# Optimization experiments

Hardware: AMD Instinct MI355X
Metric: run time of the kernel (lower is better)

The kernel has to match this reference:

```python
import jax, jax.numpy as jnp
import numpy as np

# 7 axial hex directions (dy, dx) including center, matching HexConv2d.DIRS
DIRS = [(0, 0), (1, 0), (0, 1), (-1, 1), (-1, 0), (0, -1), (1, -1)]


def _shift(x, dy, dx):
    """torch.roll-style shift with zero fill at wrapped edges. x: [B,C,H,W]."""
    sx, sy = -dx, -dy
    y = jnp.roll(x, shift=(sy, sx), axis=(2, 3))
    if sy > 0:
        y = y.at[:, :, :sy, :].set(0)
    elif sy < 0:
        y = y.at[:, :, sy:, :].set(0)
    if sx > 0:
        y = y.at[:, :, :, :sx].set(0)
    elif sx < 0:
        y = y.at[:, :, :, sx:].set(0)
    return y


def _hex_mask(H, dtype):
    size = H // 2
    q = jnp.arange(-size, size + 1)
    Q, R = jnp.meshgrid(q, q, indexing='ij')
    S = -Q - R
    # |Q|<=size and |R|<=size hold by construction; only |S|<=size cuts corners
    mask = ((jnp.abs(Q) <= size) & (jnp.abs(R) <= size) & (jnp.abs(S) <= size))
    return mask.astype(dtype)[None, None]  # [1,1,H,W]


def setup_inputs() -> dict:
    key = jax.random.key(0)
    k1, k2, k3 = jax.random.split(key, 3)
    B, Cin, Cout, H = 32, 256, 256, 49
    x = jax.random.normal(k1, (B, Cin, H, H), dtype=jnp.float32)
    weight = jax.random.normal(k2, (Cout, Cin, 7), dtype=jnp.float32) * 0.02
    bias = jax.random.normal(k3, (Cout,), dtype=jnp.float32) * 0.02
    return {"x": x, "weight": weight, "bias": bias}


def reference(x, weight, bias):
    mask = _hex_mask(x.shape[2], x.dtype)          # [1,1,H,W]
    x = x * mask
    # [7,B,C,H,W]: shifted+masked neighbor maps
    nbr = jnp.stack([_shift(x, dy, dx) for (dy, dx) in DIRS], axis=0) * mask
    # fused 1x1 conv over (channel, direction): weight [O,C,7]
    y = jnp.einsum('nbchw,ocn->bohw', nbr, weight) + bias[None, :, None, None]
    return y * mask
```

## Files before the change

### kernel.cpp

```cpp
#include <hip/hip_runtime.h>


typedef __attribute__((ext_vector_type(8))) short short8;
typedef __attribute__((ext_vector_type(4))) short short4v;
typedef __attribute__((ext_vector_type(4))) float floatx4;

#define NPIX   2401
#define W50    50
#define PREAL  2450
#define XBLEAD 56
#define XBROWS 2672
#define PT3    128
#define NT3    20
#define NSEG3  15
#define BUFB   (NSEG3*1024)
#define XB3_BYTES ((size_t)32*XBROWS*256*2)
#define WP_BYTES  917504ULL
#define WS_NEED3  (XB3_BYTES + WP_BYTES)

__device__ __forceinline__ unsigned short f2bf(float f) {
  unsigned u = __builtin_bit_cast(unsigned, f);
  u += 0x7fffu + ((u >> 16) & 1u);
  return (unsigned short)(u >> 16);
}

__global__ void prep_w_kernel(const float* __restrict__ w, unsigned short* __restrict__ wp) {
  int t = blockIdx.x * 256 + threadIdx.x;
  int l  = t & 63;
  int ot = (t >> 6) & 15;
  int kc = (t >> 10) & 7;
  int n  = t >> 13;
  int o  = ot * 16 + (l & 15);
  int cb = kc * 32 + ((l >> 4) * 8);
  const float* src = w + (size_t)(o * 256 + cb) * 7 + n;
  short8 pk;
#pragma unroll
  for (int j = 0; j < 8; ++j) pk[j] = (short)f2bf(src[j * 7]);
  ((short8*)wp)[t] = pk;
}

__global__ void zero_pads(unsigned short* __restrict__ xb) {
  int idx = blockIdx.x * 256 + threadIdx.x;
  int c16 = idx & 31;
  int rb  = idx >> 5;
  int row = rb % XBROWS;
  int b   = rb / XBROWS;
  int p   = row - XBLEAD;
  bool pad = (p < 0) || (p >= PREAL) || (p % W50 == 49);
  if (pad) {
    short8 z = {0,0,0,0,0,0,0,0};
    *(short8*)(xb + ((size_t)b * XBROWS + row) * 256 + c16 * 8) = z;
  }
}

__global__ __launch_bounds__(256)
void prep_x3(const float* __restrict__ x, unsigned short* __restrict__ xb) {
  __shared__ unsigned short t[64][68];
  const int tid = threadIdx.x;
  const int span = blockIdx.x, cg = blockIdx.y, b = blockIdx.z;
  const int s0 = span * 64;
  {
    const int chl = tid >> 2, i4 = tid & 3;
    const float* src = x + ((size_t)(b * 256 + cg * 64 + chl)) * NPIX;
#pragma unroll
    for (int it = 0; it < 4; ++it) {
      int pxl = it * 16 + i4 * 4;
      int r = s0 + pxl;
      float vv[4] = {0.f, 0.f, 0.f, 0.f};
      if (r + 3 < NPIX) {
        float4 v = *(const float4*)(src + r);
        vv[0] = v.x; vv[1] = v.y; vv[2] = v.z; vv[3] = v.w;
      } else {
#pragma unroll
        for (int e = 0; e < 4; ++e) if (r + e < NPIX) vv[e] = src[r + e];
      }
      short4v u = {0, 0, 0, 0};
#pragma unroll
      for (int e = 0; e < 4; ++e) {
        int re = r + e;
        unsigned short uu = 0;
        if (re < NPIX) {
          int h = re / 49, w = re - h * 49, s = h + w;
          if (s >= 24 && s <= 72) uu = f2bf(vv[e]);
        }
        u[e] = (short)uu;
      }
      *(short4v*)&t[chl][pxl] = u;
    }
  }
  __syncthreads();
  const int rl = tid >> 2, cpart = tid & 3;
  const int r = s0 + rl;
  if (r < NPIX) {
    int p = r + r / 49;
    unsigned short* dst = xb + ((size_t)b * XBROWS + (p + XBLEAD)) * 256 + cg * 64 + cpart * 16;
    short8 o0, o1;
#pragma unroll
    for (int k = 0; k < 8; ++k) o0[k] = (short)t[cpart * 16 + k][rl];
#pragma unroll
    for (int k = 0; k < 8; ++k) o1[k] = (short)t[cpart * 16 + 8 + k][rl];
    *(short8*)dst = o0;
    *(short8*)(dst + 8) = o1;
  }
}

__global__ __launch_bounds__(256, 2)
void hexconv_v3(const unsigned short* __restrict__ xb,
                const unsigned short* __restrict__ wp,
                const float* __restrict__ bias,
                float* __restrict__ out) {
  __shared__ __attribute__((aligned(16))) unsigned char smem[2 * BUFB];

  const int tid  = threadIdx.x;
  const int lane = tid & 63;
  const int wv   = tid >> 6;
  const int col  = lane & 15;
  const int quad = lane >> 4;

  const int pt = blockIdx.x;
  const int b  = blockIdx.y;
  const int P0 = pt * PT3;
  const int phase = (pt + b * 3) & 7;

  const int OFF[7] = {0, 50, 1, -49, -50, -1, 49};

  int ba[7];
#pragma unroll
  for (int n = 0; n < 7; ++n) {
    int r0 = col + 56 + OFF[n];
    int r64 = r0 << 6;
    ba[n] = (r64 + quad * 16) ^ ((r64 >> 3) & 0x30);
  }

  const int gpart = (lane & 3) ^ ((lane >> 3) & 3);
  const char* gsrc0 = (const char*)(xb + ((size_t)b * XBROWS + (size_t)P0) * 256)
                      + (lane >> 2) * 512 + gpart * 16;

  auto stage = [&](int buf, int kc) {
    char* ldsb = (char*)smem + buf * BUFB;
    for (int s = wv; s < NSEG3; s += 4)
      __builtin_amdgcn_global_load_lds(
          (const __attribute__((address_space(1))) unsigned int*)(gsrc0 + (size_t)s * 8192 + kc * 64),
          (__attribute__((address_space(3))) unsigned int*)(ldsb + s * 1024), 16, 0, 0);
  };

  const char* wbase = (const char*)wp + (size_t)(wv * 4) * 1024 + lane * 16;
  auto loadA = [&](int kc, int n, short8* dst) {
#pragma unroll
    for (int ii = 0; ii < 4; ++ii)
      dst[ii] = *(const short8*)(wbase + ((size_t)((n * 8 + kc) * 16 + ii)) * 1024);
  };

  floatx4 acc[4][8];
#pragma unroll
  for (int ii = 0; ii < 4; ++ii)
#pragma unroll
    for (int j = 0; j < 8; ++j) acc[ii][j] = (floatx4){0.f, 0.f, 0.f, 0.f};

  stage(0, phase);
  short8 afc[4];
  loadA(phase, 0, afc);
  __syncthreads();

  for (int i = 0; i < 8; ++i) {
    const int kc  = (i + phase) & 7;
    const int kcn = (i + 1 + phase) & 7;
    if (i < 7) stage((i + 1) & 1, kcn);
    const char* bufp = (const char*)smem + (i & 1) * BUFB;
#pragma unroll
    for (int n = 0; n < 7; ++n) {
      short8 afn[4];
      loadA((n < 6) ? kc : kcn, (n < 6) ? n + 1 : 0, afn);
      short8 bf[8];
#pragma unroll
      for (int j = 0; j < 8; ++j)
        bf[j] = *(const short8*)(bufp + ba[n] + j * 1024);
#pragma unroll
      for (int ii = 0; ii < 4; ++ii)
#pragma unroll
        for (int j = 0; j < 8; ++j)
          acc[ii][j] = __builtin_amdgcn_mfma_f32_16x16x32_bf16(afc[ii], bf[j], acc[ii][j], 0, 0, 0);
#pragma unroll
      for (int ii = 0; ii < 4; ++ii) afc[ii] = afn[ii];
    }
    __syncthreads();
  }

  const int ob = wv * 64;
  floatx4 bv[4];
#pragma unroll
  for (int ii = 0; ii < 4; ++ii)
    bv[ii] = *(const floatx4*)(bias + ob + ii * 16 + quad * 4);

#pragma unroll
  for (int j = 0; j < 8; ++j) {
    int p = P0 + j * 16 + col;
    int h = p / W50;
    int w = p - h * W50;
    if (w >= 49 || p >= PREAL) continue;
    bool m = (h + w >= 24) && (h + w <= 72);
    size_t ridx = (size_t)h * 49 + w;
#pragma unroll
    for (int ii = 0; ii < 4; ++ii) {
      float* dst = out + ((size_t)(b * 256 + ob + ii * 16 + quad * 4)) * NPIX + ridx;
#pragma unroll
      for (int rr = 0; rr < 4; ++rr) {
        float v = m ? (acc[ii][j][rr] + bv[ii][rr]) : 0.f;
        dst[(size_t)rr * NPIX] = v;
      }
    }
  }
}

#define PITCH  40
#define V1WIN  168
#define V1ZROW 168
__global__ __launch_bounds__(256)
void hexconv_v1(const float* __restrict__ x,
                const unsigned short* __restrict__ wp,
                const float* __restrict__ bias,
                float* __restrict__ out) {
  __shared__ unsigned short sm[(V1ZROW + 2) * PITCH];
  const int tid = threadIdx.x, lane = tid & 63, wv = tid >> 6;
  const int col = lane & 15, quad = lane >> 4;
  const int pt = blockIdx.x, b = blockIdx.y;
  const int P0 = pt * 64, win_start = P0 - 52;
  if (tid < PITCH * 2) sm[V1ZROW * PITCH + tid] = 0;
  const int OFF[7] = {0, 49, 1, -48, -49, -1, 48};
  const int DXP = (1 << 2) | (1 << 3), DXN = (1 << 5) | (1 << 6);
  int baddr[4][7];
#pragma unroll
  for (int j = 0; j < 4; ++j) {
    int pix = P0 + j * 16 + col;
    int wj = pix % 49;
    int rowbase = pix - win_start;
#pragma unroll
    for (int n = 0; n < 7; ++n) {
      bool bad = (((DXP >> n) & 1) && wj == 48) || (((DXN >> n) & 1) && wj == 0);
      int row = bad ? V1ZROW : (rowbase + OFF[n]);
      baddr[j][n] = row * (PITCH * 2) + quad * 16;
    }
  }
  int sp[3], sgp[3]; bool sok[3];
#pragma unroll
  for (int pi = 0; pi < 3; ++pi) {
    int p = lane + pi * 64, gp = win_start + p;
    sp[pi] = p; sgp[pi] = gp;
    bool hm = false;
    if (gp >= 0 && gp < NPIX) { int h = gp / 49, w = gp - h * 49, s = h + w; hm = (s >= 24 && s <= 72); }
    sok[pi] = (p < V1WIN) && hm;
  }
  floatx4 acc[4][4];
#pragma unroll
  for (int i = 0; i < 4; ++i)
#pragma unroll
    for (int j = 0; j < 4; ++j) acc[i][j] = (floatx4){0.f, 0.f, 0.f, 0.f};
  const short8* wpv = (const short8*)wp;
  const int wslot = wv * 4;
  for (int kc = 0; kc < 8; ++kc) {
    __syncthreads();
#pragma unroll
    for (int ci = 0; ci < 8; ++ci) {
      int c = ci * 4 + wv;
      const float* src = x + ((size_t)(b * 256 + kc * 32 + c)) * NPIX;
#pragma unroll
      for (int pi = 0; pi < 3; ++pi) {
        if (sp[pi] < V1WIN) {
          float v = sok[pi] ? src[sgp[pi]] : 0.f;
          sm[sp[pi] * PITCH + c] = f2bf(v);
        }
      }
    }
    __syncthreads();
#pragma unroll
    for (int n = 0; n < 7; ++n) {
      short8 af[4];
#pragma unroll
      for (int i = 0; i < 4; ++i)
        af[i] = wpv[((size_t)((n * 8 + kc) * 16 + wslot + i)) * 64 + lane];
      short8 bf[4];
#pragma unroll
      for (int j = 0; j < 4; ++j)
        bf[j] = *(const short8*)((const char*)sm + baddr[j][n]);
#pragma unroll
      for (int i = 0; i < 4; ++i)
#pragma unroll
        for (int j = 0; j < 4; ++j)
          acc[i][j] = __builtin_amdgcn_mfma_f32_16x16x32_bf16(af[i], bf[j], acc[i][j], 0, 0, 0);
    }
  }
  const int ob = wv * 64;
  floatx4 bv[4];
#pragma unroll
  for (int i = 0; i < 4; ++i)
    bv[i] = *(const floatx4*)(bias + ob + i * 16 + quad * 4);
#pragma unroll
  for (int j = 0; j < 4; ++j) {
    int pix = P0 + j * 16 + col;
    if (pix >= NPIX) continue;
    int h = pix / 49, w = pix - h * 49;
    bool m = (h + w >= 24 && h + w <= 72);
#pragma unroll
    for (int i = 0; i < 4; ++i) {
      int o = ob + i * 16 + quad * 4;
      float* dst = out + ((size_t)(b * 256 + o)) * NPIX + pix;
#pragma unroll
      for (int r = 0; r < 4; ++r) {
        float v = m ? (acc[i][j][r] + bv[i][r]) : 0.f;
        dst[(size_t)r * NPIX] = v;
      }
    }
  }
}

extern "C" void kernel_launch(void* const* d_in, const int* in_sizes, int n_in,
                              void* d_out, int out_size, void* d_ws, size_t ws_size,
                              hipStream_t stream) {
  const float* x    = (const float*)d_in[0];
  const float* w    = (const float*)d_in[1];
  const float* bias = (const float*)d_in[2];
  float* out = (float*)d_out;

  if (ws_size >= WS_NEED3) {
    unsigned short* xb = (unsigned short*)d_ws;
    unsigned short* wp = (unsigned short*)((char*)d_ws + XB3_BYTES);
    zero_pads<<<(32 * XBROWS * 32) / 256, 256, 0, stream>>>(xb);
    prep_w_kernel<<<224, 256, 0, stream>>>(w, wp);
    prep_x3<<<dim3(38, 4, 32), 256, 0, stream>>>(x, xb);
    hexconv_v3<<<dim3(NT3, 32), 256, 0, stream>>>(xb, wp, bias, out);
  } else {
    unsigned short* wp = (unsigned short*)d_ws;
    prep_w_kernel<<<224, 256, 0, stream>>>(w, wp);
    hexconv_v1<<<dim3(38, 32), 256, 0, stream>>>(x, wp, bias, out);
  }
}
```

Baseline: 239.0 us.

## Halve pixel tile to 64, raise occupancy, and rework prep_x transpose stores

The main conv kernel now covers 64 pixels per block instead of 128, giving 39x32 blocks. It keeps a 4x4 accumulator set, uses a smaller LDS double buffer and sets launch bounds to 3 blocks per CU. The aim is better occupancy and load balance across CUs. The cost is more redundant loading of weight and halo data per output, and the removal of the weight register prefetch. The prep_x transpose also changes so each thread packs two pixels' 8-channel vectors from 32-bit LDS reads, which targets LDS bank conflicts and wider stores.

```diff
diff --git a/kernel.cpp b/kernel.cpp
--- a/kernel.cpp
+++ b/kernel.cpp
@@ -10,10 +10,9 @@
 #define PREAL  2450
 #define XBLEAD 56
 #define XBROWS 2672
-#define PT3    128
-#define NT3    20
-#define NSEG3  15
-#define BUFB   (NSEG3*1024)
+#define NT4    39
+#define NSEG4  11
+#define BUFB4  (NSEG4*1024)
 #define XB3_BYTES ((size_t)32*XBROWS*256*2)
 #define WP_BYTES  917504ULL
 #define WS_NEED3  (XB3_BYTES + WP_BYTES)
@@ -54,7 +53,7 @@
 }
 
 __global__ __launch_bounds__(256)
-void prep_x3(const float* __restrict__ x, unsigned short* __restrict__ xb) {
+void prep_x4(const float* __restrict__ x, unsigned short* __restrict__ xb) {
   __shared__ unsigned short t[64][68];
   const int tid = threadIdx.x;
   const int span = blockIdx.x, cg = blockIdx.y, b = blockIdx.z;
@@ -62,10 +61,10 @@
   {
     const int chl = tid >> 2, i4 = tid & 3;
     const float* src = x + ((size_t)(b * 256 + cg * 64 + chl)) * NPIX;
+    const int rbase = s0 + i4 * 16;
 #pragma unroll
     for (int it = 0; it < 4; ++it) {
-      int pxl = it * 16 + i4 * 4;
-      int r = s0 + pxl;
+      int r = rbase + it * 4;
       float vv[4] = {0.f, 0.f, 0.f, 0.f};
       if (r + 3 < NPIX) {
         float4 v = *(const float4*)(src + r);
@@ -85,31 +84,44 @@
         }
         u[e] = (short)uu;
       }
-      *(short4v*)&t[chl][pxl] = u;
+      *(short4v*)&t[chl][i4 * 16 + it * 4] = u;
     }
   }
   __syncthreads();
-  const int rl = tid >> 2, cpart = tid & 3;
-  const int r = s0 + rl;
-  if (r < NPIX) {
-    int p = r + r / 49;
-    unsigned short* dst = xb + ((size_t)b * XBROWS + (p + XBLEAD)) * 256 + cg * 64 + cpart * 16;
-    short8 o0, o1;
-#pragma unroll
-    for (int k = 0; k < 8; ++k) o0[k] = (short)t[cpart * 16 + k][rl];
-#pragma unroll
-    for (int k = 0; k < 8; ++k) o1[k] = (short)t[cpart * 16 + 8 + k][rl];
-    *(short8*)dst = o0;
-    *(short8*)(dst + 8) = o1;
-  }
-}
-
-__global__ __launch_bounds__(256, 2)
-void hexconv_v3(const unsigned short* __restrict__ xb,
+  const int pp = tid >> 3;
+  const int co = tid & 7;
+  unsigned d[8];
+#pragma unroll
+  for (int k = 0; k < 8; ++k) d[k] = *(const unsigned*)&t[co * 8 + k][pp * 2];
+  uint4 lo, hi;
+  {
+    unsigned l0[4], h0[4];
+#pragma unroll
+    for (int m = 0; m < 4; ++m) {
+      unsigned a = d[2 * m], bq = d[2 * m + 1];
+      l0[m] = (a & 0xffffu) | (bq << 16);
+      h0[m] = (a >> 16) | (bq & 0xffff0000u);
+    }
+    lo = make_uint4(l0[0], l0[1], l0[2], l0[3]);
+    hi = make_uint4(h0[0], h0[1], h0[2], h0[3]);
+  }
+  const int r_lo = s0 + pp * 2, r_hi = r_lo + 1;
+  if (r_lo < NPIX) {
+    int prow = r_lo + r_lo / 49 + XBLEAD;
+    *(uint4*)(xb + ((size_t)b * XBROWS + prow) * 256 + cg * 64 + co * 8) = lo;
+  }
+  if (r_hi < NPIX) {
+    int prow = r_hi + r_hi / 49 + XBLEAD;
+    *(uint4*)(xb + ((size_t)b * XBROWS + prow) * 256 + cg * 64 + co * 8) = hi;
+  }
+}
+
+__global__ __launch_bounds__(256, 3)
+void hexconv_v4(const unsigned short* __restrict__ xb,
                 const unsigned short* __restrict__ wp,
                 const float* __restrict__ bias,
                 float* __restrict__ out) {
-  __shared__ __attribute__((aligned(16))) unsigned char smem[2 * BUFB];
+  __shared__ __attribute__((aligned(16))) unsigned char smem[2 * BUFB4];
 
   const int tid  = threadIdx.x;
   const int lane = tid & 63;
@@ -119,7 +131,7 @@
 
   const int pt = blockIdx.x;
   const int b  = blockIdx.y;
-  const int P0 = pt * PT3;
+  const int P0 = pt * 64;
   const int phase = (pt + b * 3) & 7;
 
   const int OFF[7] = {0, 50, 1, -49, -50, -1, 49};
@@ -137,51 +149,44 @@
                       + (lane >> 2) * 512 + gpart * 16;
 
   auto stage = [&](int buf, int kc) {
-    char* ldsb = (char*)smem + buf * BUFB;
-    for (int s = wv; s < NSEG3; s += 4)
+    char* ldsb = (char*)smem + buf * BUFB4;
+    for (int s = wv; s < NSEG4; s += 4)
       __builtin_amdgcn_global_load_lds(
           (const __attribute__((address_space(1))) unsigned int*)(gsrc0 + (size_t)s * 8192 + kc * 64),
           (__attribute__((address_space(3))) unsigned int*)(ldsb + s * 1024), 16, 0, 0);
   };
 
   const char* wbase = (const char*)wp + (size_t)(wv * 4) * 1024 + lane * 16;
-  auto loadA = [&](int kc, int n, short8* dst) {
-#pragma unroll
-    for (int ii = 0; ii < 4; ++ii)
-      dst[ii] = *(const short8*)(wbase + ((size_t)((n * 8 + kc) * 16 + ii)) * 1024);
-  };
-
-  floatx4 acc[4][8];
+
+  floatx4 acc[4][4];
 #pragma unroll
   for (int ii = 0; ii < 4; ++ii)
 #pragma unroll
-    for (int j = 0; j < 8; ++j) acc[ii][j] = (floatx4){0.f, 0.f, 0.f, 0.f};
+    for (int j = 0; j < 4; ++j) acc[ii][j] = (floatx4){0.f, 0.f, 0.f, 0.f};
 
   stage(0, phase);
-  short8 afc[4];
-  loadA(phase, 0, afc);
   __syncthreads();
 
   for (int i = 0; i < 8; ++i) {
     const int kc  = (i + phase) & 7;
     const int kcn = (i + 1 + phase) & 7;
     if (i < 7) stage((i + 1) & 1, kcn);
-    const char* bufp = (const char*)smem + (i & 1) * BUFB;
+    const char* bufp = (const char*)smem + (i & 1) * BUFB4;
 #pragma unroll
     for (int n = 0; n < 7; ++n) {
-      short8 afn[4];
-      loadA((n < 6) ? kc : kcn, (n < 6) ? n + 1 : 0, afn);
-      short8 bf[8];
-#pragma unroll
-      for (int j = 0; j < 8; ++j)
+      short8 af[4];
+#pragma unroll
+      for (int ii = 0; ii < 4; ++ii)
+        af[ii] = *(const short8*)(wbase + ((size_t)((n * 8 + kc) * 16 + ii)) * 1024);
+      short8 bf[4];
+#pragma unroll
+      for (int j = 0; j < 4; ++j)
         bf[j] = *(const short8*)(bufp + ba[n] + j * 1024);
 #pragma unroll
       for (int ii = 0; ii < 4; ++ii)
 #pragma unroll
-        for (int j = 0; j < 8; ++j)
-          acc[ii][j] = __builtin_amdgcn_mfma_f32_16x16x32_bf16(afc[ii], bf[j], acc[ii][j], 0, 0, 0);
-#pragma unroll
-      for (int ii = 0; ii < 4; ++ii) afc[ii] = afn[ii];
+        for (int j = 0; j < 4; ++j)
+          acc[ii][j] = __builtin_amdgcn_mfma_f32_16x16x32_bf16(af[ii], bf[j], acc[ii][j], 0, 0, 0);
     }
     __syncthreads();
   }
@@ -193,7 +198,7 @@
     bv[ii] = *(const floatx4*)(bias + ob + ii * 16 + quad * 4);
 
 #pragma unroll
-  for (int j = 0; j < 8; ++j) {
+  for (int j = 0; j < 4; ++j) {
     int p = P0 + j * 16 + col;
     int h = p / W50;
     int w = p - h * W50;
@@ -326,8 +331,8 @@
     unsigned short* wp = (unsigned short*)((char*)d_ws + XB3_BYTES);
     zero_pads<<<(32 * XBROWS * 32) / 256, 256, 0, stream>>>(xb);
     prep_w_kernel<<<224, 256, 0, stream>>>(w, wp);
-    prep_x3<<<dim3(38, 4, 32), 256, 0, stream>>>(x, xb);
-    hexconv_v3<<<dim3(NT3, 32), 256, 0, stream>>>(xb, wp, bias, out);
+    prep_x4<<<dim3(38, 4, 32), 256, 0, stream>>>(x, xb);
+    hexconv_v4<<<dim3(NT4, 32), 256, 0, stream>>>(xb, wp, bias, out);
   } else {
     unsigned short* wp = (unsigned short*)d_ws;
     prep_w_kernel<<<224, 256, 0, stream>>>(w, wp);
```

Measured after the change: 265.0 us. +10.9%, slower.
